# Kernel optimization log

Hardware: AMD Instinct MI355X
Metric: run time of the kernel (lower is better)

The kernel has to match this reference:

```python
import jax, jax.numpy as jnp
import numpy as np

N, E = 50000, 800000
EMB, HEADS, EDGE_DIM = 64, 4, 16
NEG_SLOPE = 0.2
LN_EPS = 1e-5


def setup_inputs() -> dict:
    key = jax.random.key(0)
    ks = jax.random.split(key, 12)
    HC = HEADS * EMB
    inp = {
        'x': jax.random.normal(ks[0], (N, EMB), jnp.float32),
        'edge_index': jax.random.randint(ks[1], (2, E), 0, N, jnp.int32),
        'edge_attr': jax.random.normal(ks[2], (E, EDGE_DIM), jnp.float32),
        # GATConv params
        'W': jax.random.normal(ks[3], (EMB, HC), jnp.float32) * 0.1,
        'W_edge': jax.random.normal(ks[4], (EDGE_DIM, HC), jnp.float32) * 0.1,
        'att_src': jax.random.normal(ks[5], (HEADS, EMB), jnp.float32) * 0.1,
        'att_dst': jax.random.normal(ks[6], (HEADS, EMB), jnp.float32) * 0.1,
        'att_edge': jax.random.normal(ks[7], (HEADS, EMB), jnp.float32) * 0.1,
        'bias': jnp.zeros((HC,), jnp.float32),
        # projection Linear(heads*emb -> emb)
        'Wp': jax.random.normal(ks[8], (HC, EMB), jnp.float32) * 0.05,
        'bp': jnp.zeros((EMB,), jnp.float32),
        # LayerNorm
        'gamma': jnp.ones((EMB,), jnp.float32),
        'beta': jnp.zeros((EMB,), jnp.float32),
    }
    return inp


def reference(x, edge_index, edge_attr, W, W_edge, att_src, att_dst, att_edge,
              bias, Wp, bp, gamma, beta):
    n = x.shape[0]
    H, C = att_src.shape

    # node transform (shared lin for src/dst since in_channels is an int)
    xw = (x @ W).reshape(n, H, C)                       # [N,H,C]
    a_src_n = jnp.einsum('nhc,hc->nh', xw, att_src)     # [N,H]
    a_dst_n = jnp.einsum('nhc,hc->nh', xw, att_dst)

    src, dst = edge_index[0], edge_index[1]

    # add self loops; fill_value='mean' -> loop edge_attr = mean of incoming edge_attr per node
    loop = jnp.arange(n, dtype=edge_index.dtype)
    cnt = jax.ops.segment_sum(jnp.ones_like(dst, jnp.float32), dst, num_segments=n)
    loop_attr = jax.ops.segment_sum(edge_attr, dst, num_segments=n) / jnp.maximum(cnt, 1.0)[:, None]
    src2 = jnp.concatenate([src, loop])
    dst2 = jnp.concatenate([dst, loop])
    ea = jnp.concatenate([edge_attr, loop_attr], axis=0)  # [E+N,edge_dim]

    ew = (ea @ W_edge).reshape(-1, H, C)                 # [E+N,H,C]
    a_edge = jnp.einsum('ehc,hc->eh', ew, att_edge)      # [E+N,H]

    alpha = a_src_n[src2] + a_dst_n[dst2] + a_edge       # [E+N,H]
    alpha = jnp.where(alpha >= 0, alpha, NEG_SLOPE * alpha)  # leaky_relu(0.2)

    # segment softmax over dst neighborhoods (self loops guarantee non-empty)
    amax = jax.ops.segment_max(alpha, dst2, num_segments=n)
    ae = jnp.exp(alpha - amax[dst2])
    denom = jax.ops.segment_sum(ae, dst2, num_segments=n)
    attn = ae / denom[dst2]                              # [E+N,H]

    msg = xw[src2] * attn[:, :, None]                    # [E+N,H,C]
    agg = jax.ops.segment_sum(msg, dst2, num_segments=n) # [N,H,C]
    gat_out = agg.reshape(n, H * C) + bias               # concat heads + bias

    proj = gat_out @ Wp + bp
    h = x + jax.nn.elu(proj)                             # residual

    mu = jnp.mean(h, axis=-1, keepdims=True)
    var = jnp.mean((h - mu) ** 2, axis=-1, keepdims=True)
    out = (h - mu) * jax.lax.rsqrt(var + LN_EPS) * gamma + beta
    return out
```

## Files before the change

### kernel.cpp

```cpp
#include <hip/hip_runtime.h>
#include <hip/hip_bf16.h>
#include <hip/hip_fp8.h>
#include <math.h>

#define EMB 64
#define HEADS 4
#define HC 256
#define EDGE_DIM 16
#define NEG_SLOPE 0.2f
#define LN_EPS 1e-5f
#define NCOLS 272
#define CAP 512
#define NPB 16

typedef __attribute__((ext_vector_type(8))) short short8;
typedef __attribute__((ext_vector_type(4))) float f32x4;
typedef __attribute__((ext_vector_type(2))) float f32x2;

__device__ __forceinline__ float bflo(unsigned int u) { return __uint_as_float(u << 16); }
__device__ __forceinline__ float bfhi(unsigned int u) { return __uint_as_float(u & 0xffff0000u); }
__device__ __forceinline__ unsigned short bfb(float f) {
    __hip_bfloat16 h = __float2bfloat16(f);
    return *(unsigned short*)&h;
}
__device__ __forceinline__ unsigned int pack_bf2(float a, float b) {
    return (unsigned int)bfb(a) | ((unsigned int)bfb(b) << 16);
}
__device__ __forceinline__ unsigned char ftofp8(float f) {
    __hip_fp8_e4m3 t(f); return (unsigned char)t.__x;
}

__global__ void k_prep(const float* __restrict__ W_edge, const float* __restrict__ att_edge,
                       float* __restrict__ we_att, const float* __restrict__ Wp,
                       unsigned short* __restrict__ WpT, const float* __restrict__ W,
                       const float* __restrict__ att_src, const float* __restrict__ att_dst,
                       unsigned short* __restrict__ WxT, int* __restrict__ cnt, int n) {
    int i = blockIdx.x * blockDim.x + threadIdx.x;
    if (i < n) cnt[i] = 0;
    if (i < EDGE_DIM * HEADS) {
        int d = i >> 2, h = i & 3;
        float acc = 0.0f;
#pragma unroll
        for (int c = 0; c < EMB; ++c)
            acc += W_edge[d * HC + h * EMB + c] * att_edge[h * EMB + c];
        we_att[d * HEADS + h] = acc;
    }
    if (i < HC * EMB) {
        int k = i >> 8, jj = i & 255;
        WpT[i] = bfb(Wp[jj * EMB + k]);
    }
    if (i < NCOLS * EMB) {
        int c = i >> 6, k = i & 63;
        float v = 0.0f;
        if (c < HC) {
            v = W[k * HC + c];
        } else if (c < HC + 4) {
            int h = c - HC;
            float s = 0.0f;
#pragma unroll
            for (int j = 0; j < EMB; ++j) s += W[k * HC + h * EMB + j] * att_src[h * EMB + j];
            v = s;
        } else if (c < HC + 8) {
            int h = c - HC - 4;
            float s = 0.0f;
#pragma unroll
            for (int j = 0; j < EMB; ++j) s += W[k * HC + h * EMB + j] * att_dst[h * EMB + j];
            v = s;
        }
        WxT[i] = bfb(v);
    }
}

__global__ void __launch_bounds__(256)
k_xw_mfma(const float* __restrict__ x, const unsigned short* __restrict__ WxT,
          unsigned char* __restrict__ xwf8, float* __restrict__ a_src,
          float* __restrict__ a_dst, int n,
          const int* __restrict__ ei, int* __restrict__ cnt,
          int* __restrict__ rank, int E) {
    int tid = threadIdx.x, lane = tid & 63, wv = tid >> 6;
    int g = lane >> 4, r16 = lane & 15;
    int mbase = blockIdx.x * 16;
    int row = mbase + r16;
    if (row >= n) row = n - 1;

    const float* xr = x + (size_t)row * EMB;
    short8 A[2];
#pragma unroll
    for (int kk = 0; kk < 2; ++kk) {
        float4 f0 = *(const float4*)(xr + kk * 32 + 8 * g);
        float4 f1 = *(const float4*)(xr + kk * 32 + 8 * g + 4);
        short8 a;
        a[0] = (short)bfb(f0.x); a[1] = (short)bfb(f0.y);
        a[2] = (short)bfb(f0.z); a[3] = (short)bfb(f0.w);
        a[4] = (short)bfb(f1.x); a[5] = (short)bfb(f1.y);
        a[6] = (short)bfb(f1.z); a[7] = (short)bfb(f1.w);
        A[kk] = a;
    }

    for (int t = wv; t <= 16; t += 4) {
        int col = t * 16 + r16;
        const unsigned short* bp = WxT + (size_t)col * EMB + 8 * g;
        short8 B0 = *(const short8*)(bp);
        short8 B1 = *(const short8*)(bp + 32);
        f32x4 acc = {0.f, 0.f, 0.f, 0.f};
        acc = __builtin_amdgcn_mfma_f32_16x16x32_bf16(A[0], B0, acc, 0, 0, 0);
        acc = __builtin_amdgcn_mfma_f32_16x16x32_bf16(A[1], B1, acc, 0, 0, 0);
        if (t < 16) {
#pragma unroll
            for (int r = 0; r < 4; ++r) {
                int node = mbase + 4 * g + r;
                if (node < n) xwf8[(size_t)node * HC + col] = ftofp8(acc[r]);
            }
        } else {
#pragma unroll
            for (int r = 0; r < 4; ++r) {
                int node = mbase + 4 * g + r;
                if (node < n) {
                    if (r16 < 4) a_src[node * HEADS + r16] = acc[r];
                    else if (r16 < 8) a_dst[node * HEADS + r16 - 4] = acc[r];
                }
            }
        }
    }

    int stride = gridDim.x * blockDim.x;
    for (int e = blockIdx.x * blockDim.x + tid; e < E; e += stride)
        rank[e] = atomicAdd(&cnt[ei[E + e]], 1);
}

__global__ void k_scan1(const int* __restrict__ cnt, int* __restrict__ tmp,
                        int* __restrict__ bsum, int n) {
    __shared__ int s[256];
    int i = blockIdx.x * 256 + threadIdx.x;
    int v = (i < n) ? cnt[i] : 0;
    s[threadIdx.x] = v;
    __syncthreads();
    for (int off = 1; off < 256; off <<= 1) {
        int t = (threadIdx.x >= off) ? s[threadIdx.x - off] : 0;
        __syncthreads();
        s[threadIdx.x] += t;
        __syncthreads();
    }
    if (i < n) tmp[i] = s[threadIdx.x];
    if (threadIdx.x == 255) bsum[blockIdx.x] = s[255];
}

__global__ void k_scan2(int* __restrict__ bsum, int nb) {
    __shared__ int s[256];
    int v = (threadIdx.x < nb) ? bsum[threadIdx.x] : 0;
    s[threadIdx.x] = v;
    __syncthreads();
    for (int off = 1; off < 256; off <<= 1) {
        int t = (threadIdx.x >= off) ? s[threadIdx.x - off] : 0;
        __syncthreads();
        s[threadIdx.x] += t;
        __syncthreads();
    }
    if (threadIdx.x < nb) bsum[threadIdx.x] = s[threadIdx.x] - v;
}

__global__ void k_scan3(const int* __restrict__ tmp, const int* __restrict__ cnt,
                        const int* __restrict__ bsum, int* __restrict__ row_start, int n) {
    int i = blockIdx.x * 256 + threadIdx.x;
    if (i < n) row_start[i] = tmp[i] - cnt[i] + bsum[blockIdx.x];
}

__global__ void k_scatter(const int* __restrict__ ei, const float* __restrict__ edge_attr,
                          const float* __restrict__ we_att, const float* __restrict__ a_src,
                          const float* __restrict__ a_dst, const int* __restrict__ row_start,
                          const int* __restrict__ rank, uint4* __restrict__ recp, int E) {
    __shared__ float wa[EDGE_DIM * HEADS];
    if (threadIdx.x < EDGE_DIM * HEADS) wa[threadIdx.x] = we_att[threadIdx.x];
    __syncthreads();
    int e = blockIdx.x * blockDim.x + threadIdx.x;
    if (e >= E) return;
    int s = ei[e], d = ei[E + e];
    const float4* ea4 = (const float4*)(edge_attr + (size_t)e * EDGE_DIM);
    float ae[HEADS] = {0.f, 0.f, 0.f, 0.f};
#pragma unroll
    for (int q = 0; q < 4; ++q) {
        float4 v4 = ea4[q];
        const float* vp = (const float*)&v4;
#pragma unroll
        for (int r = 0; r < 4; ++r) {
            float v = vp[r];
            int dd = q * 4 + r;
#pragma unroll
            for (int h = 0; h < HEADS; ++h) ae[h] += v * wa[dd * HEADS + h];
        }
    }
    float4 as4 = *(const float4*)(a_src + (size_t)s * HEADS);
    float4 ad4 = *(const float4*)(a_dst + (size_t)d * HEADS);
    const float* asp = (const float*)&as4;
    const float* adp = (const float*)&ad4;
    float ea[HEADS];
    unsigned int aeq = 0;
#pragma unroll
    for (int h = 0; h < HEADS; ++h) {
        float al = asp[h] + adp[h] + ae[h];
        al = al >= 0.0f ? al : NEG_SLOPE * al;
        ea[h] = __expf(al);
        int q = __float2int_rn(ae[h] * 32.0f);
        q = max(-127, min(127, q));
        aeq |= ((unsigned int)(q & 0xff)) << (8 * h);
    }
    int pos = row_start[d] + rank[e];
    uint4 w;
    w.x = pack_bf2(ea[0], ea[1]);
    w.y = pack_bf2(ea[2], ea[3]);
    w.z = (unsigned int)s;
    w.w = aeq;
    recp[pos] = w;
}

template<int D>
__device__ __forceinline__ void gather_batch(
    const uint4* recs, int o, int j, const unsigned char* xwf8, int lane,
    int h4, bool hodd, int sh1,
    float& acc0, float& acc1, float& acc2, float& acc3, float& dn, float& aeS) {
    int sv[D];
#pragma unroll
    for (int u = 0; u < D; ++u) sv[u] = (int)recs[o + j + u].z;
    unsigned int rv[D];
#pragma unroll
    for (int u = 0; u < D; ++u)
        rv[u] = *(const unsigned int*)(xwf8 + (size_t)sv[u] * HC + (lane << 2));
#pragma unroll
    for (int u = 0; u < D; ++u) {
        uint4 W = recs[o + j + u];
        unsigned sel = (h4 & 2) ? W.y : W.x;
        float a = hodd ? bfhi(sel) : bflo(sel);
        aeS += (float)((int)(W.w << sh1) >> 24);
        dn += a;
        f32x2 lo2 = __builtin_amdgcn_cvt_pk_f32_fp8((int)rv[u], false);
        f32x2 hi2 = __builtin_amdgcn_cvt_pk_f32_fp8((int)rv[u], true);
        acc0 += a * lo2.x; acc1 += a * lo2.y;
        acc2 += a * hi2.x; acc3 += a * hi2.y;
    }
}

__device__ __forceinline__ void node_range(
    const uint4* recs, int o, int c, const unsigned char* xwf8, int lane,
    int h4, bool hodd, int sh1,
    float& acc0, float& acc1, float& acc2, float& acc3, float& dn, float& aeS) {
    int j = 0;
    for (; j + 8 <= c; j += 8)
        gather_batch<8>(recs, o, j, xwf8, lane, h4, hodd, sh1, acc0, acc1, acc2, acc3, dn, aeS);
    if (j + 4 <= c) {
        gather_batch<4>(recs, o, j, xwf8, lane, h4, hodd, sh1, acc0, acc1, acc2, acc3, dn, aeS);
        j += 4;
    }
    for (; j < c; ++j)
        gather_batch<1>(recs, o, j, xwf8, lane, h4, hodd, sh1, acc0, acc1, acc2, acc3, dn, aeS);
}

#define LDS_BYTES (NPB * 272 * 2 + NPB * 66 * 4)
__global__ void __launch_bounds__(256)
k_gather_out(const int* __restrict__ row_start, const int* __restrict__ cnt,
             const uint4* __restrict__ recp,
             const float* __restrict__ a_src, const float* __restrict__ a_dst,
             const unsigned char* __restrict__ xwf8, const float* __restrict__ x,
             const float* __restrict__ bias, const unsigned short* __restrict__ WpT,
             const float* __restrict__ bp, const float* __restrict__ gamma,
             const float* __restrict__ beta, float* __restrict__ out, int n) {
    int tid = threadIdx.x, lane = tid & 63, wv = tid >> 6;
    int h4 = lane >> 4;
    bool hodd = (h4 & 1);
    int sh1 = (3 - h4) * 8;

    __shared__ __align__(16) unsigned char ldsbuf[LDS_BYTES];
    uint4* recs = (uint4*)ldsbuf;
    unsigned short (*gbf)[272] = (unsigned short (*)[272])ldsbuf;
    float (*pC)[66] = (float (*)[66])(ldsbuf + NPB * 272 * 2);

    int first = blockIdx.x * NPB;
    int last = min(first + NPB, n) - 1;
    int rs0 = row_start[first];
    int total = row_start[last] + cnt[last] - rs0;

    int nd[4], dgq[4], mLo[4], mHi[4];
#pragma unroll
    for (int q = 0; q < 4; ++q) {
        int node = first + wv * 4 + q;
        bool v = node < n;
        int nc = v ? node : n - 1;
        nd[q] = nc;
        dgq[q] = v ? cnt[nc] : 0;
        mLo[q] = row_start[nc] - rs0;
        mHi[q] = mLo[q] + dgq[q];
    }

    float a00 = 0.f, a01 = 0.f, a02 = 0.f, a03 = 0.f, dn0 = 0.f, ae0 = 0.f;
    float a10 = 0.f, a11 = 0.f, a12 = 0.f, a13 = 0.f, dn1 = 0.f, ae1 = 0.f;
    float a20 = 0.f, a21 = 0.f, a22 = 0.f, a23 = 0.f, dn2 = 0.f, ae2 = 0.f;
    float a30 = 0.f, a31 = 0.f, a32 = 0.f, a33 = 0.f, dn3 = 0.f, ae3 = 0.f;

    for (int base = 0; base < total; base += CAP) {
        int cend = min(total, base + CAP);
        if (base) __syncthreads();
        for (int idx = base + tid; idx < cend; idx += 256)
            recs[idx - base] = recp[rs0 + idx];
        __syncthreads();
        {
            int lo = max(mLo[0], base), hi = min(mHi[0], cend);
            if (hi > lo) node_range(recs, lo - base, hi - lo, xwf8, lane, h4, hodd, sh1,
                                    a00, a01, a02, a03, dn0, ae0);
        }
        {
            int lo = max(mLo[1], base), hi = min(mHi[1], cend);
            if (hi > lo) node_range(recs, lo - base, hi - lo, xwf8, lane, h4, hodd, sh1,
                                    a10, a11, a12, a13, dn1, ae1);
        }
        {
            int lo = max(mLo[2], base), hi = min(mHi[2], cend);
            if (hi > lo) node_range(recs, lo - base, hi - lo, xwf8, lane, h4, hodd, sh1,
                                    a20, a21, a22, a23, dn2, ae2);
        }
        {
            int lo = max(mLo[3], base), hi = min(mHi[3], cend);
            if (hi > lo) node_range(recs, lo - base, hi - lo, xwf8, lane, h4, hodd, sh1,
                                    a30, a31, a32, a33, dn3, ae3);
        }
    }
    __syncthreads();

    float4 bv = *(const float4*)(bias + (lane << 2));
#pragma unroll
    for (int q = 0; q < 4; ++q) {
        float A0 = (q == 0) ? a00 : (q == 1) ? a10 : (q == 2) ? a20 : a30;
        float A1 = (q == 0) ? a01 : (q == 1) ? a11 : (q == 2) ? a21 : a31;
        float A2 = (q == 0) ? a02 : (q == 1) ? a12 : (q == 2) ? a22 : a32;
        float A3 = (q == 0) ? a03 : (q == 1) ? a13 : (q == 2) ? a23 : a33;
        float DN = (q == 0) ? dn0 : (q == 1) ? dn1 : (q == 2) ? dn2 : dn3;
        float AE = (q == 0) ? ae0 : (q == 1) ? ae1 : (q == 2) ? ae2 : ae3;
        int nc = nd[q];
        float as = a_src[nc * HEADS + h4];
        float ad = a_dst[nc * HEADS + h4];
        unsigned int sr8 = *(const unsigned int*)(xwf8 + (size_t)nc * HC + (lane << 2));
        float cf = fmaxf((float)dgq[q], 1.0f);
        float al = as + ad + (AE * (1.0f / 32.0f)) / cf;
        al = al >= 0.f ? al : NEG_SLOPE * al;
        float el = __expf(al);
        float inv = 1.0f / (DN + el);
        f32x2 slo = __builtin_amdgcn_cvt_pk_f32_fp8((int)sr8, false);
        f32x2 shi = __builtin_amdgcn_cvt_pk_f32_fp8((int)sr8, true);
        ushort4 gv;
        gv.x = bfb((A0 + el * slo.x) * inv + bv.x);
        gv.y = bfb((A1 + el * slo.y) * inv + bv.y);
        gv.z = bfb((A2 + el * shi.x) * inv + bv.z);
        gv.w = bfb((A3 + el * shi.y) * inv + bv.w);
        *(ushort4*)&gbf[wv * 4 + q][lane << 2] = gv;
    }
    __syncthreads();

    {
        int g = lane >> 4, r16 = lane & 15;
        const unsigned short* wp = WpT + (size_t)(wv * 16 + r16) * HC + 8 * g;
        const unsigned short* ga = &gbf[r16][8 * g];
        f32x4 pacc = {0.f, 0.f, 0.f, 0.f};
#pragma unroll
        for (int kk = 0; kk < 8; ++kk) {
            short8 Af = *(const short8*)(ga + kk * 32);
            short8 Bf = *(const short8*)(wp + kk * 32);
            pacc = __builtin_amdgcn_mfma_f32_16x16x32_bf16(Af, Bf, pacc, 0, 0, 0);
        }
#pragma unroll
        for (int m = 0; m < 4; ++m) pC[4 * g + m][wv * 16 + r16] = pacc[m];
    }
    __syncthreads();

#pragma unroll
    for (int p = 0; p < 4; ++p) {
        int local = wv + 4 * p;
        int node = first + local;
        bool v2 = node < n;
        float pv = pC[local][lane] + bp[lane];
        float elv = pv > 0.f ? pv : expm1f(pv);
        float xv = v2 ? x[(size_t)node * EMB + lane] : 0.f;
        float hv = xv + elv;
        float s1 = hv, s2 = hv * hv;
        for (int off = 32; off > 0; off >>= 1) {
            s1 += __shfl_xor(s1, off);
            s2 += __shfl_xor(s2, off);
        }
        float mu = s1 * (1.0f / EMB);
        float var = s2 * (1.0f / EMB) - mu * mu;
        if (v2)
            out[(size_t)node * EMB + lane] =
                (hv - mu) * rsqrtf(var + LN_EPS) * gamma[lane] + beta[lane];
    }
}

extern "C" void kernel_launch(void* const* d_in, const int* in_sizes, int n_in,
                              void* d_out, int out_size, void* d_ws, size_t ws_size,
                              hipStream_t stream) {
    const float* x        = (const float*)d_in[0];
    const int*   ei       = (const int*)d_in[1];
    const float* edge_attr= (const float*)d_in[2];
    const float* W        = (const float*)d_in[3];
    const float* W_edge   = (const float*)d_in[4];
    const float* att_src  = (const float*)d_in[5];
    const float* att_dst  = (const float*)d_in[6];
    const float* att_edge = (const float*)d_in[7];
    const float* bias     = (const float*)d_in[8];
    const float* Wp       = (const float*)d_in[9];
    const float* bp       = (const float*)d_in[10];
    const float* gamma    = (const float*)d_in[11];
    const float* beta     = (const float*)d_in[12];
    float* out = (float*)d_out;

    int n = in_sizes[0] / EMB;
    int E = in_sizes[1] / 2;
    int nb = (n + 255) / 256;

    float* ws = (float*)d_ws;
    float* a_src       = ws; ws += (size_t)n * HEADS;
    float* a_dst       = ws; ws += (size_t)n * HEADS;
    float* we_att      = ws; ws += EDGE_DIM * HEADS;
    unsigned char* xwf8 = (unsigned char*)ws; ws += (size_t)n * HC / 4;
    uint4* recp        = (uint4*)ws; ws += (size_t)E * 4;
    unsigned short* WpT = (unsigned short*)ws; ws += HC * EMB / 2;
    unsigned short* WxT = (unsigned short*)ws; ws += NCOLS * EMB / 2;
    int* iw = (int*)ws;
    int* cnt       = iw; iw += n;
    int* rank      = iw; iw += E;
    int* row_start = iw; iw += n;
    int* tmp       = iw; iw += n;
    int* bsum      = iw; iw += 256;

    const int tb = 256;
    hipLaunchKernelGGL(k_prep, dim3((n + tb - 1) / tb), dim3(tb), 0, stream,
                       W_edge, att_edge, we_att, Wp, WpT, W, att_src, att_dst, WxT, cnt, n);
    hipLaunchKernelGGL(k_xw_mfma, dim3((n + 15) / 16), dim3(tb), 0, stream,
                       x, WxT, xwf8, a_src, a_dst, n, ei, cnt, rank, E);
    hipLaunchKernelGGL(k_scan1, dim3(nb), dim3(tb), 0, stream, cnt, tmp, bsum, n);
    hipLaunchKernelGGL(k_scan2, dim3(1), dim3(tb), 0, stream, bsum, nb);
    hipLaunchKernelGGL(k_scan3, dim3(nb), dim3(tb), 0, stream, tmp, cnt, bsum, row_start, n);
    hipLaunchKernelGGL(k_scatter, dim3((E + tb - 1) / tb), dim3(tb), 0, stream,
                       ei, edge_attr, we_att, a_src, a_dst, row_start, rank, recp, E);
    hipLaunchKernelGGL(k_gather_out, dim3((n + NPB - 1) / NPB), dim3(tb), 0, stream,
                       row_start, cnt, recp, a_src, a_dst, xwf8, x, bias, WpT, bp,
                       gamma, beta, out, n);
}
```

Before: 152.9 us.

## Shrink gather kernel to single-wave blocks of four nodes without barriers

The gather/output kernel now launches one 64-thread wavefront per block, handling 4 nodes instead of 16, so every __syncthreads is replaced by LDS waitcnt fences. The projection MFMA is restructured so one wave computes all 64 output columns, looping over four weight tiles and reusing the loaded A fragments. This removes cross-wave barrier stalls and lets blocks with skewed degree finish independently. In exchange, 12 of the 16 MFMA rows are wasted and the Wp weights are reloaded four times as often per node.

```diff
diff --git a/kernel.cpp b/kernel.cpp
--- a/kernel.cpp
+++ b/kernel.cpp
@@ -10,8 +10,8 @@
 #define NEG_SLOPE 0.2f
 #define LN_EPS 1e-5f
 #define NCOLS 272
-#define CAP 512
-#define NPB 16
+#define CAP 128
+#define NPB 4
 
 typedef __attribute__((ext_vector_type(8))) short short8;
 typedef __attribute__((ext_vector_type(4))) float f32x4;
@@ -255,7 +255,7 @@
 }
 
 #define LDS_BYTES (NPB * 272 * 2 + NPB * 66 * 4)
-__global__ void __launch_bounds__(256)
+__global__ void __launch_bounds__(64)
 k_gather_out(const int* __restrict__ row_start, const int* __restrict__ cnt,
              const uint4* __restrict__ recp,
              const float* __restrict__ a_src, const float* __restrict__ a_dst,
@@ -263,7 +263,7 @@
              const float* __restrict__ bias, const unsigned short* __restrict__ WpT,
              const float* __restrict__ bp, const float* __restrict__ gamma,
              const float* __restrict__ beta, float* __restrict__ out, int n) {
-    int tid = threadIdx.x, lane = tid & 63, wv = tid >> 6;
+    int lane = threadIdx.x;
     int h4 = lane >> 4;
     bool hodd = (h4 & 1);
     int sh1 = (3 - h4) * 8;
@@ -281,7 +281,7 @@
     int nd[4], dgq[4], mLo[4], mHi[4];
 #pragma unroll
     for (int q = 0; q < 4; ++q) {
-        int node = first + wv * 4 + q;
+        int node = first + q;
         bool v = node < n;
         int nc = v ? node : n - 1;
         nd[q] = nc;
@@ -297,10 +297,9 @@
 
     for (int base = 0; base < total; base += CAP) {
         int cend = min(total, base + CAP);
-        if (base) __syncthreads();
-        for (int idx = base + tid; idx < cend; idx += 256)
+        for (int idx = base + lane; idx < cend; idx += 64)
             recs[idx - base] = recp[rs0 + idx];
-        __syncthreads();
+        asm volatile("s_waitcnt lgkmcnt(0)" ::: "memory");
         {
             int lo = max(mLo[0], base), hi = min(mHi[0], cend);
             if (hi > lo) node_range(recs, lo - base, hi - lo, xwf8, lane, h4, hodd, sh1,
@@ -321,8 +320,9 @@
             if (hi > lo) node_range(recs, lo - base, hi - lo, xwf8, lane, h4, hodd, sh1,
                                     a30, a31, a32, a33, dn3, ae3);
         }
-    }
-    __syncthreads();
+        asm volatile("" ::: "memory");
+    }
+    asm volatile("s_waitcnt lgkmcnt(0)" ::: "memory");
 
     float4 bv = *(const float4*)(bias + (lane << 2));
 #pragma unroll
@@ -349,32 +349,38 @@
         gv.y = bfb((A1 + el * slo.y) * inv + bv.y);
         gv.z = bfb((A2 + el * shi.x) * inv + bv.z);
         gv.w = bfb((A3 + el * shi.y) * inv + bv.w);
-        *(ushort4*)&gbf[wv * 4 + q][lane << 2] = gv;
-    }
-    __syncthreads();
+        *(ushort4*)&gbf[q][lane << 2] = gv;
+    }
+    asm volatile("s_waitcnt lgkmcnt(0)" ::: "memory");
 
     {
         int g = lane >> 4, r16 = lane & 15;
-        const unsigned short* wp = WpT + (size_t)(wv * 16 + r16) * HC + 8 * g;
-        const unsigned short* ga = &gbf[r16][8 * g];
-        f32x4 pacc = {0.f, 0.f, 0.f, 0.f};
-#pragma unroll
-        for (int kk = 0; kk < 8; ++kk) {
-            short8 Af = *(const short8*)(ga + kk * 32);
-            short8 Bf = *(const short8*)(wp + kk * 32);
-            pacc = __builtin_amdgcn_mfma_f32_16x16x32_bf16(Af, Bf, pacc, 0, 0, 0);
-        }
-#pragma unroll
-        for (int m = 0; m < 4; ++m) pC[4 * g + m][wv * 16 + r16] = pacc[m];
-    }
-    __syncthreads();
+        const unsigned short* ga = &gbf[r16 & 3][8 * g];
+        short8 Af[8];
+#pragma unroll
+        for (int kk = 0; kk < 8; ++kk) Af[kk] = *(const short8*)(ga + kk * 32);
+#pragma unroll
+        for (int t = 0; t < 4; ++t) {
+            const unsigned short* wp = WpT + (size_t)(t * 16 + r16) * HC + 8 * g;
+            f32x4 pacc = {0.f, 0.f, 0.f, 0.f};
+#pragma unroll
+            for (int kk = 0; kk < 8; ++kk) {
+                short8 Bf = *(const short8*)(wp + kk * 32);
+                pacc = __builtin_amdgcn_mfma_f32_16x16x32_bf16(Af[kk], Bf, pacc, 0, 0, 0);
+            }
+            if (g == 0) {
+#pragma unroll
+                for (int m = 0; m < 4; ++m) pC[m][t * 16 + r16] = pacc[m];
+            }
+        }
+    }
+    asm volatile("s_waitcnt lgkmcnt(0)" ::: "memory");
 
 #pragma unroll
     for (int p = 0; p < 4; ++p) {
-        int local = wv + 4 * p;
-        int node = first + local;
+        int node = first + p;
         bool v2 = node < n;
-        float pv = pC[local][lane] + bp[lane];
+        float pv = pC[p][lane] + bp[lane];
         float elv = pv > 0.f ? pv : expm1f(pv);
         float xv = v2 ? x[(size_t)node * EMB + lane] : 0.f;
         float hv = xv + elv;
@@ -438,7 +444,7 @@
     hipLaunchKernelGGL(k_scan3, dim3(nb), dim3(tb), 0, stream, tmp, cnt, bsum, row_start, n);
     hipLaunchKernelGGL(k_scatter, dim3((E + tb - 1) / tb), dim3(tb), 0, stream,
                        ei, edge_attr, we_att, a_src, a_dst, row_start, rank, recp, E);
-    hipLaunchKernelGGL(k_gather_out, dim3((n + NPB - 1) / NPB), dim3(tb), 0, stream,
+    hipLaunchKernelGGL(k_gather_out, dim3((n + NPB - 1) / NPB), dim3(64), 0, stream,
                        row_start, cnt, recp, a_src, a_dst, xwf8, x, bias, WpT, bp,
                        gamma, beta, out, n);
 }
```

New measurement: 166.2 us. +8.7%, slower.
